# Kernel optimization log

Measured on AMD Instinct MI355X. Metric: run time of the kernel, lower is better.

## Reference

```python
import jax, jax.numpy as jnp
import numpy as np

D_MODEL = 256
OUT_DIM = 256
D_STATE = 16
D_CONV = 4
EXPAND = 2
D_INNER = EXPAND * D_MODEL  # 512
DT_RANK = (D_MODEL + 15) // 16  # 16
B_SZ, L = 2, 4096


def setup_inputs() -> dict:
    key = jax.random.key(0)
    ks = jax.random.split(key, 12)
    s = lambda *sh: 0.02
    inp = {}
    inp['x'] = jax.random.normal(ks[0], (B_SZ, L, D_MODEL), jnp.float32)
    inp['ln_w'] = jnp.ones((D_MODEL,), jnp.float32)
    inp['ln_b'] = jnp.zeros((D_MODEL,), jnp.float32)
    inp['in_proj_w'] = jax.random.normal(ks[1], (2 * D_INNER, D_MODEL), jnp.float32) * 0.02
    inp['conv_w'] = jax.random.normal(ks[2], (D_INNER, 1, D_CONV), jnp.float32) * 0.2
    inp['conv_b'] = jnp.zeros((D_INNER,), jnp.float32)
    inp['x_proj_w'] = jax.random.normal(ks[3], (DT_RANK + 2 * D_STATE, D_INNER), jnp.float32) * 0.02
    inp['dt_proj_w'] = jax.random.normal(ks[4], (D_INNER, DT_RANK), jnp.float32) * 0.05
    inp['dt_proj_b'] = jax.random.uniform(ks[5], (D_INNER,), jnp.float32, -4.0, -2.0)  # small dt after softplus
    inp['A_log'] = jnp.log(jnp.broadcast_to(jnp.arange(1, D_STATE + 1, dtype=jnp.float32), (D_INNER, D_STATE)))
    inp['Dskip'] = jnp.ones((D_INNER,), jnp.float32)
    inp['out_proj_w'] = jax.random.normal(ks[6], (D_MODEL, D_INNER), jnp.float32) * 0.02
    inp['proj_w'] = jax.random.normal(ks[7], (OUT_DIM, D_MODEL), jnp.float32) * 0.02
    inp['proj_b'] = jnp.zeros((OUT_DIM,), jnp.float32)
    inp['skip_scale'] = jnp.ones((1,), jnp.float32)
    return inp


def _layernorm(x, w, b, eps=1e-5):
    mu = jnp.mean(x, axis=-1, keepdims=True)
    var = jnp.var(x, axis=-1, keepdims=True)
    return (x - mu) * jax.lax.rsqrt(var + eps) * w + b


def _selective_scan(u, delta, A, Bm, Cm, Dskip):
    # u, delta: (B,L,d); A: (d,n); Bm, Cm: (B,L,n)
    dA = jnp.exp(delta[..., None] * A)                       # (B,L,d,n)
    dBu = (delta * u)[..., None] * Bm[:, :, None, :]          # (B,L,d,n)
    h0 = jnp.zeros((u.shape[0], A.shape[0], A.shape[1]), u.dtype)

    def step(h, inp):
        dA_t, dBu_t, C_t = inp
        h = dA_t * h + dBu_t                                  # (B,d,n)
        y = jnp.einsum('bdn,bn->bd', h, C_t)
        return h, y

    xs = (dA.transpose(1, 0, 2, 3), dBu.transpose(1, 0, 2, 3), Cm.transpose(1, 0, 2))
    _, ys = jax.lax.scan(step, h0, xs)                        # (L,B,d)
    return ys.transpose(1, 0, 2) + u * Dskip


def _mamba(xn, in_proj_w, conv_w, conv_b, x_proj_w, dt_proj_w, dt_proj_b, A_log, Dskip, out_proj_w):
    # xn: (B,L,d_model)
    xz = jnp.einsum('bld,ed->ble', xn, in_proj_w)             # (B,L,2*d_inner)
    xi, z = jnp.split(xz, 2, axis=-1)
    # depthwise causal conv over L
    xc = jax.lax.conv_general_dilated(
        xi.transpose(0, 2, 1), conv_w, window_strides=(1,),
        padding=[(D_CONV - 1, 0)], feature_group_count=D_INNER,
        dimension_numbers=('NCH', 'OIH', 'NCH'))
    xc = (xc + conv_b[None, :, None]).transpose(0, 2, 1)       # (B,L,d_inner)
    xc = jax.nn.silu(xc)
    dbc = jnp.einsum('bld,ed->ble', xc, x_proj_w)             # (B,L,dt_rank+2n)
    dt, Bm, Cm = jnp.split(dbc, [DT_RANK, DT_RANK + D_STATE], axis=-1)
    delta = jax.nn.softplus(jnp.einsum('blr,dr->bld', dt, dt_proj_w) + dt_proj_b)
    A = -jnp.exp(A_log)                                       # (d_inner, n)
    y = _selective_scan(xc, delta, A, Bm, Cm, Dskip)
    y = y * jax.nn.silu(z)
    return jnp.einsum('ble,de->bld', y, out_proj_w)


def reference(x, ln_w, ln_b, in_proj_w, conv_w, conv_b, x_proj_w, dt_proj_w, dt_proj_b,
              A_log, Dskip, out_proj_w, proj_w, proj_b, skip_scale):
    x_norm = _layernorm(x, ln_w, ln_b)
    x_mamba = _mamba(x_norm, in_proj_w, conv_w, conv_b, x_proj_w, dt_proj_w, dt_proj_b,
                     A_log, Dskip, out_proj_w) + skip_scale * x
    x_mamba = _layernorm(x_mamba, ln_w, ln_b)
    return jnp.einsum('bld,od->blo', x_mamba, proj_w) + proj_b
```

## Files before the change

### kernel.cpp

```cpp
#include <hip/hip_runtime.h>
#include <hip/hip_bf16.h>

#define B_SZ   2
#define LSEQ   4096
#define NCH    512
#define CL     8
#define DROWS  16

typedef __attribute__((ext_vector_type(8))) short short8;
typedef __attribute__((ext_vector_type(4))) float f32x4;

__device__ __forceinline__ unsigned short f2bf(float f) {
  union { float f; unsigned u; } x; x.f = f;
  unsigned r = x.u + 0x7fffu + ((x.u >> 16) & 1u);
  return (unsigned short)(r >> 16);
}
__device__ __forceinline__ float bf2f(unsigned short u) {
  union { unsigned u; float f; } x; x.u = (unsigned)u << 16;
  return x.f;
}

__device__ __forceinline__ void gload_lds16(const unsigned short* g, unsigned short* l) {
  __builtin_amdgcn_global_load_lds(
      (const __attribute__((address_space(1))) unsigned int*)g,
      (__attribute__((address_space(3))) unsigned int*)l, 16, 0, 0);
}

__global__ __launch_bounds__(256) void prep_kernel(
    const float* __restrict__ x, const float* __restrict__ ln_w,
    const float* __restrict__ ln_b, unsigned short* __restrict__ xn_bf,
    const float* __restrict__ inW,  unsigned short* __restrict__ inW_bf,
    const float* __restrict__ outW, unsigned short* __restrict__ outW_bf,
    const float* __restrict__ projW, unsigned short* __restrict__ projW_bf,
    const float* __restrict__ xprojW, unsigned short* __restrict__ xprojW_bf,
    const float* __restrict__ A_log, float* __restrict__ Ar_tab)
{
  if (blockIdx.x < 2048) {
    int wv = threadIdx.x >> 6, lane = threadIdx.x & 63;
    size_t row = (size_t)blockIdx.x * 4 + wv;
    float4 v = reinterpret_cast<const float4*>(x)[row * 64 + lane];
    float s  = v.x + v.y + v.z + v.w;
    float sq = v.x*v.x + v.y*v.y + v.z*v.z + v.w*v.w;
    #pragma unroll
    for (int off = 32; off; off >>= 1) {
      s  += __shfl_xor(s,  off);
      sq += __shfl_xor(sq, off);
    }
    float mu  = s * (1.f/256.f);
    float var = sq * (1.f/256.f) - mu*mu;
    float rs  = rsqrtf(var + 1e-5f);
    float4 wv4 = reinterpret_cast<const float4*>(ln_w)[lane];
    float4 bv4 = reinterpret_cast<const float4*>(ln_b)[lane];
    ushort4 o;
    o.x = f2bf((v.x-mu)*rs*wv4.x + bv4.x);
    o.y = f2bf((v.y-mu)*rs*wv4.y + bv4.y);
    o.z = f2bf((v.z-mu)*rs*wv4.z + bv4.z);
    o.w = f2bf((v.w-mu)*rs*wv4.w + bv4.w);
    reinterpret_cast<ushort4*>(xn_bf)[row * 64 + lane] = o;
    return;
  }
  int j = (blockIdx.x - 2048) * 256 + threadIdx.x;
  const float* src; unsigned short* dst; int off;
  if (j < 65536)       { src = inW;    dst = inW_bf;    off = j; }
  else if (j < 98304)  { src = outW;   dst = outW_bf;   off = j - 65536; }
  else if (j < 114688) { src = projW;  dst = projW_bf;  off = j - 98304; }
  else if (j < 120832) { src = xprojW; dst = xprojW_bf; off = j - 114688; }
  else {
    int a = (j - 120832) * 4;
    float4 v = *reinterpret_cast<const float4*>(A_log + a);
    float4 o = {-__expf(v.x), -__expf(v.y), -__expf(v.z), -__expf(v.w)};
    *reinterpret_cast<float4*>(Ar_tab + a) = o;
    return;
  }
  float4 v = *reinterpret_cast<const float4*>(src + off*4);
  ushort4 o;
  o.x = f2bf(v.x); o.y = f2bf(v.y); o.z = f2bf(v.z); o.w = f2bf(v.w);
  *reinterpret_cast<ushort4*>(dst + off*4) = o;
}

__global__ __launch_bounds__(256) void ln_bf16_kernel(
    const unsigned short* __restrict__ in, const float* __restrict__ w,
    const float* __restrict__ b, unsigned short* __restrict__ out)
{
  int wv = threadIdx.x >> 6, lane = threadIdx.x & 63;
  size_t row = (size_t)blockIdx.x * 4 + wv;
  ushort4 uv = reinterpret_cast<const ushort4*>(in)[row * 64 + lane];
  float4 v = {bf2f(uv.x), bf2f(uv.y), bf2f(uv.z), bf2f(uv.w)};
  float s  = v.x + v.y + v.z + v.w;
  float sq = v.x*v.x + v.y*v.y + v.z*v.z + v.w*v.w;
  #pragma unroll
  for (int off = 32; off; off >>= 1) {
    s  += __shfl_xor(s,  off);
    sq += __shfl_xor(sq, off);
  }
  float mu  = s * (1.f/256.f);
  float var = sq * (1.f/256.f) - mu*mu;
  float rs  = rsqrtf(var + 1e-5f);
  float4 wv4 = reinterpret_cast<const float4*>(w)[lane];
  float4 bv4 = reinterpret_cast<const float4*>(b)[lane];
  ushort4 o;
  o.x = f2bf((v.x-mu)*rs*wv4.x + bv4.x);
  o.y = f2bf((v.y-mu)*rs*wv4.y + bv4.y);
  o.z = f2bf((v.z-mu)*rs*wv4.z + bv4.z);
  o.w = f2bf((v.w-mu)*rs*wv4.w + bv4.w);
  reinterpret_cast<ushort4*>(out)[row * 64 + lane] = o;
}

enum { EPI_NONE = 0, EPI_SKIPX = 1, EPI_BIAS = 2 };

template<int BM, int BN, int EPI, typename OT>
__global__ __launch_bounds__(256) void gemm_mfma(
    const unsigned short* __restrict__ A, const unsigned short* __restrict__ W,
    OT* __restrict__ C, int M, int N, int K,
    const float* __restrict__ X, const float* __restrict__ sscale,
    const float* __restrict__ bias)
{
  constexpr int BK = 32;
  constexpr int WM = BM / 2, WN = BN / 2;
  constexpr int AM = WM / 16, BF = WN / 16;
  constexpr int AI = BM / 64, BI = BN / 64;
  __shared__ __align__(16) unsigned short As[2][BM * BK];
  __shared__ __align__(16) unsigned short Ws[2][BN * BK];
  const int tid = threadIdx.x, lane = tid & 63, wid = tid >> 6;
  const int wr = wid >> 1, wc = wid & 1;
  const int bm = blockIdx.x * BM, bn = blockIdx.y * BN;
  const int srow = lane >> 2;
  const int skoff = (lane & 3) * 8;

  f32x4 acc[AM][BF] = {};

  auto stage = [&](int buf, int kt) {
    #pragma unroll
    for (int i = 0; i < AI; i++) {
      int rowg = (wid * AI + i) * 16;
      gload_lds16(A + (size_t)(bm + rowg + srow) * K + kt + skoff,
                  &As[buf][rowg * BK]);
    }
    #pragma unroll
    for (int i = 0; i < BI; i++) {
      int rowg = (wid * BI + i) * 16;
      gload_lds16(W + (size_t)(bn + rowg + srow) * K + kt + skoff,
                  &Ws[buf][rowg * BK]);
    }
  };

  stage(0, 0);
  __syncthreads();
  const int nt = K / BK;
  int cur = 0;
  for (int t = 0; t < nt; t++) {
    if (t + 1 < nt) stage(cur ^ 1, (t + 1) * BK);
    short8 af[AM], bfr[BF];
    #pragma unroll
    for (int i = 0; i < AM; i++)
      af[i] = *reinterpret_cast<const short8*>(
          &As[cur][(wr * WM + i * 16 + (lane & 15)) * BK + (lane >> 4) * 8]);
    #pragma unroll
    for (int j = 0; j < BF; j++)
      bfr[j] = *reinterpret_cast<const short8*>(
          &Ws[cur][(wc * WN + j * 16 + (lane & 15)) * BK + (lane >> 4) * 8]);
    #pragma unroll
    for (int i = 0; i < AM; i++)
      #pragma unroll
      for (int j = 0; j < BF; j++)
        acc[i][j] = __builtin_amdgcn_mfma_f32_16x16x32_bf16(af[i], bfr[j], acc[i][j], 0, 0, 0);
    __syncthreads();
    cur ^= 1;
  }

  float sv = 0.f;
  if constexpr (EPI == EPI_SKIPX) sv = sscale[0];

  #pragma unroll
  for (int i = 0; i < AM; i++) {
    #pragma unroll
    for (int j = 0; j < BF; j++) {
      int row0 = bm + wr * WM + i * 16 + ((lane >> 4) << 2);
      int col  = bn + wc * WN + j * 16 + (lane & 15);
      #pragma unroll
      for (int r = 0; r < 4; r++) {
        float v = acc[i][j][r];
        size_t off = (size_t)(row0 + r) * N + col;
        if constexpr (EPI == EPI_SKIPX) v += sv * X[off];
        if constexpr (EPI == EPI_BIAS)  v += bias[col];
        if constexpr (sizeof(OT) == 2) C[off] = (OT)f2bf(v);
        else                           C[off] = v;
      }
    }
  }
}

__global__ __launch_bounds__(256) void gemm_mfma48(
    const unsigned short* __restrict__ A, const unsigned short* __restrict__ W,
    float* __restrict__ C, int K)
{
  __shared__ __align__(16) unsigned short As[2][64 * 32];
  __shared__ __align__(16) unsigned short Ws[2][48 * 32];
  const int tid = threadIdx.x, lane = tid & 63, wid = tid >> 6;
  const int bm = blockIdx.x * 64;
  const int srow = lane >> 2, skoff = (lane & 3) * 8;

  f32x4 acc[3] = {};

  auto stage = [&](int buf, int kt) {
    int rowg = wid * 16;
    gload_lds16(A + (size_t)(bm + rowg + srow) * K + kt + skoff, &As[buf][rowg * 32]);
    if (wid < 3)
      gload_lds16(W + (size_t)(rowg + srow) * K + kt + skoff, &Ws[buf][rowg * 32]);
  };

  stage(0, 0);
  __syncthreads();
  const int nt = K / 32;
  int cur = 0;
  for (int t = 0; t < nt; t++) {
    if (t + 1 < nt) stage(cur ^ 1, (t + 1) * 32);
    short8 af = *reinterpret_cast<const short8*>(
        &As[cur][(wid * 16 + (lane & 15)) * 32 + (lane >> 4) * 8]);
    #pragma unroll
    for (int j = 0; j < 3; j++) {
      short8 bfr = *reinterpret_cast<const short8*>(
          &Ws[cur][(j * 16 + (lane & 15)) * 32 + (lane >> 4) * 8]);
      acc[j] = __builtin_amdgcn_mfma_f32_16x16x32_bf16(af, bfr, acc[j], 0, 0, 0);
    }
    __syncthreads();
    cur ^= 1;
  }
  int row0 = bm + wid * 16 + ((lane >> 4) << 2);
  #pragma unroll
  for (int j = 0; j < 3; j++) {
    int col = j * 16 + (lane & 15);
    #pragma unroll
    for (int r = 0; r < 4; r++)
      C[(size_t)(row0 + r) * 48 + col] = acc[j][r];
  }
}

__global__ __launch_bounds__(256) void conv_silu_kernel(
    const unsigned short* __restrict__ xz, const float* __restrict__ cw,
    const float* __restrict__ cb, unsigned short* __restrict__ xc_bf)
{
  int idx = blockIdx.x * 256 + threadIdx.x;
  int d4 = (idx & 127) << 2;
  int bt = idx >> 7;
  int t  = bt & (LSEQ - 1);
  int b  = bt >> 12;
  float a0 = cb[d4], a1 = cb[d4+1], a2 = cb[d4+2], a3 = cb[d4+3];
  float4 w0 = *reinterpret_cast<const float4*>(&cw[(d4+0)*4]);
  float4 w1 = *reinterpret_cast<const float4*>(&cw[(d4+1)*4]);
  float4 w2 = *reinterpret_cast<const float4*>(&cw[(d4+2)*4]);
  float4 w3 = *reinterpret_cast<const float4*>(&cw[(d4+3)*4]);
  const float* wp0 = (const float*)&w0;
  const float* wp1 = (const float*)&w1;
  const float* wp2 = (const float*)&w2;
  const float* wp3 = (const float*)&w3;
  #pragma unroll
  for (int j = 0; j < 4; j++) {
    int tt = t - 3 + j;
    if (tt >= 0) {
      ushort4 xv = *reinterpret_cast<const ushort4*>(&xz[((size_t)b*LSEQ + tt)*1024 + d4]);
      a0 += wp0[j]*bf2f(xv.x); a1 += wp1[j]*bf2f(xv.y);
      a2 += wp2[j]*bf2f(xv.z); a3 += wp3[j]*bf2f(xv.w);
    }
  }
  ushort4 ob;
  ob.x = f2bf(a0 / (1.f + __expf(-a0)));
  ob.y = f2bf(a1 / (1.f + __expf(-a1)));
  ob.z = f2bf(a2 / (1.f + __expf(-a2)));
  ob.w = f2bf(a3 / (1.f + __expf(-a3)));
  *reinterpret_cast<ushort4*>(&xc_bf[((size_t)b*LSEQ + t)*512 + d4]) = ob;
}

__global__ __launch_bounds__(256) void dtproj2_kernel(
    const float* __restrict__ dbc, const float* __restrict__ dpw,
    const float* __restrict__ dpb, unsigned short* __restrict__ delta_bf)
{
  const int tid = threadIdx.x;
  const int d0 = (tid & 127) << 2;
  float4 w[4][4];
  #pragma unroll
  for (int dd = 0; dd < 4; dd++) {
    const float4* wr = reinterpret_cast<const float4*>(&dpw[(d0+dd)*16]);
    w[dd][0] = wr[0]; w[dd][1] = wr[1]; w[dd][2] = wr[2]; w[dd][3] = wr[3];
  }
  float4 bias = *reinterpret_cast<const float4*>(&dpb[d0]);
  const float* bp = (const float*)&bias;
  size_t rbase = (size_t)blockIdx.x * DROWS + (tid >> 7);
  #pragma unroll 2
  for (int rr = 0; rr < DROWS; rr += 2) {
    size_t r = rbase + rr;
    const float4* dt = reinterpret_cast<const float4*>(dbc + r*48);
    float4 t0 = dt[0], t1 = dt[1], t2 = dt[2], t3 = dt[3];
    ushort4 ob;
    unsigned short* obp = (unsigned short*)&ob;
    #pragma unroll
    for (int dd = 0; dd < 4; dd++) {
      float acc = bp[dd];
      acc += t0.x*w[dd][0].x + t0.y*w[dd][0].y + t0.z*w[dd][0].z + t0.w*w[dd][0].w;
      acc += t1.x*w[dd][1].x + t1.y*w[dd][1].y + t1.z*w[dd][1].z + t1.w*w[dd][1].w;
      acc += t2.x*w[dd][2].x + t2.y*w[dd][2].y + t2.z*w[dd][2].z + t2.w*w[dd][2].w;
      acc += t3.x*w[dd][3].x + t3.y*w[dd][3].y + t3.z*w[dd][3].z + t3.w*w[dd][3].w;
      obp[dd] = f2bf(fmaxf(acc, 0.f) + log1pf(__expf(-fabsf(acc))));
    }
    *reinterpret_cast<ushort4*>(&delta_bf[r*512 + d0]) = ob;
  }
}

__global__ __launch_bounds__(256) void scanA_kernel(
    const unsigned short* __restrict__ delta_bf, const unsigned short* __restrict__ xc_bf,
    const float* __restrict__ dbc, const float* __restrict__ Ar_tab,
    unsigned short* __restrict__ hloc, float* __restrict__ Ssum)
{
  __shared__ float Bs[CL][16];
  const int tid = threadIdx.x;
  int g = blockIdx.x * 256 + tid;
  int nh = g & 1;
  int d  = (g >> 1) & 511;
  int c  = (g >> 10) & (NCH - 1);
  int b  = g >> 19;
  size_t tbase = (size_t)b * LSEQ + (size_t)c * CL;
  if (tid < CL * 16)
    Bs[tid >> 4][tid & 15] = dbc[(tbase + (tid >> 4)) * 48 + 16 + (tid & 15)];
  const float4* Ap = reinterpret_cast<const float4*>(Ar_tab + d*16 + nh*8);
  float4 A0 = Ap[0], A1 = Ap[1];
  float Ar[8] = {A0.x, A0.y, A0.z, A0.w, A1.x, A1.y, A1.z, A1.w};
  float h[8] = {};
  float S = 0.f;
  __syncthreads();
  #pragma unroll
  for (int t = 0; t < CL; t++) {
    size_t r = tbase + t;
    float dl = bf2f(delta_bf[r*512 + d]);
    float u  = bf2f(xc_bf[r*512 + d]);
    float du = dl * u;
    S += dl;
    float4 B0 = *reinterpret_cast<const float4*>(&Bs[t][nh*8]);
    float4 B1 = *reinterpret_cast<const float4*>(&Bs[t][nh*8 + 4]);
    float Bv[8] = {B0.x,B0.y,B0.z,B0.w, B1.x,B1.y,B1.z,B1.w};
    #pragma unroll
    for (int n = 0; n < 8; n++)
      h[n] = __expf(dl * Ar[n]) * h[n] + du * Bv[n];
  }
  size_t o = (((size_t)c * B_SZ + b) * 512 + d) * 16 + nh*8;
  short8 hs;
  #pragma unroll
  for (int n = 0; n < 8; n++) hs[n] = (short)f2bf(h[n]);
  *reinterpret_cast<short8*>(&hloc[o]) = hs;
  if (nh == 0) Ssum[((size_t)c * B_SZ + b) * 512 + d] = S;
}

__global__ __launch_bounds__(256) void scanmid2_kernel(
    const unsigned short* __restrict__ hloc, const float* __restrict__ Ssum,
    const float* __restrict__ Ar_tab, unsigned short* __restrict__ henter)
{
  int g = blockIdx.x * 256 + threadIdx.x;
  int n = g & 15, d = (g >> 4) & 511, b = g >> 13;
  float Ar = Ar_tab[d*16 + n];
  float h = 0.f;
  #pragma unroll 4
  for (int c = 0; c < NCH; c++) {
    size_t idx = ((size_t)c * B_SZ + b) * 512 + d;
    henter[idx*16 + n] = f2bf(h);
    h = __expf(Ssum[idx] * Ar) * h + bf2f(hloc[idx*16 + n]);
  }
}

__global__ __launch_bounds__(256) void scanB_kernel(
    const unsigned short* __restrict__ delta_bf, const unsigned short* __restrict__ xc_bf,
    const float* __restrict__ dbc, const float* __restrict__ Ar_tab,
    const unsigned short* __restrict__ henter, const float* __restrict__ Dskip,
    const unsigned short* __restrict__ xz, unsigned short* __restrict__ y_bf)
{
  __shared__ float Bs[CL][16];
  __shared__ float Cs[CL][16];
  const int tid = threadIdx.x;
  int g = blockIdx.x * 256 + tid;
  int nh = g & 1;
  int d  = (g >> 1) & 511;
  int c  = (g >> 10) & (NCH - 1);
  int b  = g >> 19;
  size_t tbase = (size_t)b * LSEQ + (size_t)c * CL;
  if (tid < CL * 16) {
    int ts = tid >> 4, is = tid & 15;
    Bs[ts][is] = dbc[(tbase + ts) * 48 + 16 + is];
  } else if (tid < 2 * CL * 16) {
    int t2 = tid - CL * 16;
    int ts = t2 >> 4, is = t2 & 15;
    Cs[ts][is] = dbc[(tbase + ts) * 48 + 32 + is];
  }
  const float4* Ap = reinterpret_cast<const float4*>(Ar_tab + d*16 + nh*8);
  float4 A0 = Ap[0], A1 = Ap[1];
  float Ar[8] = {A0.x, A0.y, A0.z, A0.w, A1.x, A1.y, A1.z, A1.w};
  size_t o = (((size_t)c * B_SZ + b) * 512 + d) * 16 + nh*8;
  short8 hv = *reinterpret_cast<const short8*>(&henter[o]);
  float h[8];
  #pragma unroll
  for (int n = 0; n < 8; n++) h[n] = bf2f((unsigned short)hv[n]);
  float Dsk = Dskip[d];
  __syncthreads();
  #pragma unroll
  for (int t = 0; t < CL; t++) {
    size_t r = tbase + t;
    float dl = bf2f(delta_bf[r*512 + d]);
    float u  = bf2f(xc_bf[r*512 + d]);
    float du = dl * u;
    float4 B0 = *reinterpret_cast<const float4*>(&Bs[t][nh*8]);
    float4 B1 = *reinterpret_cast<const float4*>(&Bs[t][nh*8 + 4]);
    float4 C0 = *reinterpret_cast<const float4*>(&Cs[t][nh*8]);
    float4 C1 = *reinterpret_cast<const float4*>(&Cs[t][nh*8 + 4]);
    float Bv[8] = {B0.x,B0.y,B0.z,B0.w, B1.x,B1.y,B1.z,B1.w};
    float Cv[8] = {C0.x,C0.y,C0.z,C0.w, C1.x,C1.y,C1.z,C1.w};
    float yp = 0.f;
    #pragma unroll
    for (int n = 0; n < 8; n++) {
      h[n] = __expf(dl * Ar[n]) * h[n] + du * Bv[n];
      yp += h[n] * Cv[n];
    }
    float y = yp + __shfl_xor(yp, 1);
    if (nh == 0) {
      y += u * Dsk;
      float z = bf2f(xz[r*1024 + 512 + d]);
      float sig = 1.f / (1.f + __expf(-z));
      y_bf[r*512 + d] = f2bf(y * z * sig);
    }
  }
}

extern "C" void kernel_launch(void* const* d_in, const int* in_sizes, int n_in,
                              void* d_out, int out_size, void* d_ws, size_t ws_size,
                              hipStream_t stream)
{
  const float* x      = (const float*)d_in[0];
  const float* ln_w   = (const float*)d_in[1];
  const float* ln_b   = (const float*)d_in[2];
  const float* inW    = (const float*)d_in[3];
  const float* convW  = (const float*)d_in[4];
  const float* convB  = (const float*)d_in[5];
  const float* xprojW = (const float*)d_in[6];
  const float* dtW    = (const float*)d_in[7];
  const float* dtB    = (const float*)d_in[8];
  const float* A_log  = (const float*)d_in[9];
  const float* Dskip  = (const float*)d_in[10];
  const float* outW   = (const float*)d_in[11];
  const float* projW  = (const float*)d_in[12];
  const float* projB  = (const float*)d_in[13];
  const float* skip   = (const float*)d_in[14];
  float* out = (float*)d_out;

  const size_t BL = (size_t)B_SZ * LSEQ;
  char* p = (char*)d_ws;
  unsigned short* xn_bf = (unsigned short*)p;  p += BL*256*2;
  unsigned short* xz_bf = (unsigned short*)p;  p += BL*1024*2;
  unsigned short* xc_bf = (unsigned short*)p;  p += BL*512*2;
  float* dbc    = (float*)p;                   p += BL*48*4;
  unsigned short* delta_bf = (unsigned short*)p; p += BL*512*2;
  unsigned short* hloc   = (unsigned short*)p; p += (size_t)NCH*B_SZ*512*16*2;
  unsigned short* henter = (unsigned short*)p; p += (size_t)NCH*B_SZ*512*16*2;
  float* Ssum   = (float*)p;                   p += (size_t)NCH*B_SZ*512*4;
  unsigned short* y_bf = (unsigned short*)p;   p += BL*512*2;
  unsigned short* inW_bf  = (unsigned short*)p; p += 1024*256*2;
  unsigned short* outW_bf = (unsigned short*)p; p += 256*512*2;
  unsigned short* projW_bf= (unsigned short*)p; p += 256*256*2;
  unsigned short* xprojW_bf=(unsigned short*)p; p += 48*512*2;
  float* Ar_tab = (float*)p;                   p += 512*16*4;
  unsigned short* xm_bf  = hloc;
  unsigned short* xn2_bf = xn_bf;

  prep_kernel<<<2048 + 480, 256, 0, stream>>>(
      x, ln_w, ln_b, xn_bf, inW, inW_bf, outW, outW_bf,
      projW, projW_bf, xprojW, xprojW_bf, A_log, Ar_tab);

  gemm_mfma<128,128,EPI_NONE><<<dim3(BL/128, 1024/128), 256, 0, stream>>>(
      xn_bf, inW_bf, xz_bf, (int)BL, 1024, 256, nullptr, nullptr, nullptr);

  conv_silu_kernel<<<(B_SZ*LSEQ*128)/256, 256, 0, stream>>>(xz_bf, convW, convB, xc_bf);

  gemm_mfma48<<<BL/64, 256, 0, stream>>>(xc_bf, xprojW_bf, dbc, 512);

  dtproj2_kernel<<<BL/DROWS, 256, 0, stream>>>(dbc, dtW, dtB, delta_bf);

  scanA_kernel<<<(B_SZ*NCH*512*2)/256, 256, 0, stream>>>(
      delta_bf, xc_bf, dbc, Ar_tab, hloc, Ssum);
  scanmid2_kernel<<<B_SZ*512*16/256, 256, 0, stream>>>(hloc, Ssum, Ar_tab, henter);
  scanB_kernel<<<(B_SZ*NCH*512*2)/256, 256, 0, stream>>>(
      delta_bf, xc_bf, dbc, Ar_tab, henter, Dskip, xz_bf, y_bf);

  gemm_mfma<64,64,EPI_SKIPX><<<dim3(BL/64, 256/64), 256, 0, stream>>>(
      y_bf, outW_bf, xm_bf, (int)BL, 256, 512, x, skip, nullptr);

  ln_bf16_kernel<<<BL/4, 256, 0, stream>>>(xm_bf, ln_w, ln_b, xn2_bf);

  gemm_mfma<64,64,EPI_BIAS><<<dim3(BL/64, 256/64), 256, 0, stream>>>(
      xn2_bf, projW_bf, out, (int)BL, 256, 256, nullptr, nullptr, projB);
}
```

Measured before the change: 255.9 us.

## Split sequential chunk-carry scan into three-level hierarchical scan across chunk groups

The middle scan over 512 chunks used to run as one serial loop per (b,d,n), launched as only 64 blocks. It now runs in three stages: per-group decay/value aggregates computed in parallel over 16 groups, a short 16-step carry scan across groups, and a per-group pass that writes entering states. This exposes about 16x more parallelism and shortens the serial dependency chain. The cost is two extra kernel launches, extra float workspace, and rereading hloc and Ssum twice.

```diff
diff --git a/kernel.cpp b/kernel.cpp
--- a/kernel.cpp
+++ b/kernel.cpp
@@ -5,6 +5,8 @@
 #define LSEQ   4096
 #define NCH    512
 #define CL     8
+#define NG     16
+#define GC     (NCH/NG)
 #define DROWS  16
 
 typedef __attribute__((ext_vector_type(8))) short short8;
@@ -349,16 +351,61 @@
   if (nh == 0) Ssum[((size_t)c * B_SZ + b) * 512 + d] = S;
 }
 
-__global__ __launch_bounds__(256) void scanmid2_kernel(
+__global__ __launch_bounds__(256) void scanmidA_kernel(
     const unsigned short* __restrict__ hloc, const float* __restrict__ Ssum,
-    const float* __restrict__ Ar_tab, unsigned short* __restrict__ henter)
+    const float* __restrict__ Ar_tab, float* __restrict__ Eg, float* __restrict__ Vg)
+{
+  int blk = blockIdx.x;
+  int dblk = blk & 31;
+  int grp  = (blk >> 5) & (NG - 1);
+  int b    = blk >> 9;
+  int n  = threadIdx.x & 15, dlo = threadIdx.x >> 4;
+  int d  = dblk * 16 + dlo;
+  float Ar = Ar_tab[d*16 + n];
+  float E = 1.f, V = 0.f;
+  #pragma unroll 4
+  for (int i = 0; i < GC; i++) {
+    int c = grp * GC + i;
+    size_t idx = ((size_t)c * B_SZ + b) * 512 + d;
+    float Ec = __expf(Ssum[idx] * Ar);
+    V = Ec * V + bf2f(hloc[idx*16 + n]);
+    E *= Ec;
+  }
+  size_t o = (size_t)grp * (B_SZ*8192) + (size_t)b * 8192 + d*16 + n;
+  Eg[o] = E;
+  Vg[o] = V;
+}
+
+__global__ __launch_bounds__(256) void scanmidB_kernel(
+    const float* __restrict__ Eg, const float* __restrict__ Vg,
+    float* __restrict__ Gent)
 {
   int g = blockIdx.x * 256 + threadIdx.x;
-  int n = g & 15, d = (g >> 4) & 511, b = g >> 13;
+  float h = 0.f;
+  #pragma unroll
+  for (int grp = 0; grp < NG; grp++) {
+    size_t o = (size_t)grp * (B_SZ*8192) + g;
+    Gent[o] = h;
+    h = Eg[o] * h + Vg[o];
+  }
+}
+
+__global__ __launch_bounds__(256) void scanmidC_kernel(
+    const unsigned short* __restrict__ hloc, const float* __restrict__ Ssum,
+    const float* __restrict__ Ar_tab, const float* __restrict__ Gent,
+    unsigned short* __restrict__ henter)
+{
+  int blk = blockIdx.x;
+  int dblk = blk & 31;
+  int grp  = (blk >> 5) & (NG - 1);
+  int b    = blk >> 9;
+  int n  = threadIdx.x & 15, dlo = threadIdx.x >> 4;
+  int d  = dblk * 16 + dlo;
   float Ar = Ar_tab[d*16 + n];
-  float h = 0.f;
+  float h = Gent[(size_t)grp * (B_SZ*8192) + (size_t)b * 8192 + d*16 + n];
   #pragma unroll 4
-  for (int c = 0; c < NCH; c++) {
+  for (int i = 0; i < GC; i++) {
+    int c = grp * GC + i;
     size_t idx = ((size_t)c * B_SZ + b) * 512 + d;
     henter[idx*16 + n] = f2bf(h);
     h = __expf(Ssum[idx] * Ar) * h + bf2f(hloc[idx*16 + n]);
@@ -463,6 +510,9 @@
   unsigned short* projW_bf= (unsigned short*)p; p += 256*256*2;
   unsigned short* xprojW_bf=(unsigned short*)p; p += 48*512*2;
   float* Ar_tab = (float*)p;                   p += 512*16*4;
+  float* Eg     = (float*)p;                   p += (size_t)NG*B_SZ*8192*4;
+  float* Vg     = (float*)p;                   p += (size_t)NG*B_SZ*8192*4;
+  float* Gent   = (float*)p;                   p += (size_t)NG*B_SZ*8192*4;
   unsigned short* xm_bf  = hloc;
   unsigned short* xn2_bf = xn_bf;
 
@@ -481,7 +531,9 @@
 
   scanA_kernel<<<(B_SZ*NCH*512*2)/256, 256, 0, stream>>>(
       delta_bf, xc_bf, dbc, Ar_tab, hloc, Ssum);
-  scanmid2_kernel<<<B_SZ*512*16/256, 256, 0, stream>>>(hloc, Ssum, Ar_tab, henter);
+  scanmidA_kernel<<<B_SZ*NG*32, 256, 0, stream>>>(hloc, Ssum, Ar_tab, Eg, Vg);
+  scanmidB_kernel<<<B_SZ*8192/256, 256, 0, stream>>>(Eg, Vg, Gent);
+  scanmidC_kernel<<<B_SZ*NG*32, 256, 0, stream>>>(hloc, Ssum, Ar_tab, Gent, henter);
   scanB_kernel<<<(B_SZ*NCH*512*2)/256, 256, 0, stream>>>(
       delta_bf, xc_bf, dbc, Ar_tab, henter, Dskip, xz_bf, y_bf);
 
```

After: 217.8 us, median of 2. -14.9%, faster.
